# Kernel tuning notes

Hardware: AMD Instinct MI355X
Metric: run time of the kernel (lower is better)

Reference implementation:

```python
import jax, jax.numpy as jnp
import numpy as np

N_NODES = 100000
N_EDGES = 3200000
N_GRAPHS = 512
F_IN = 128
HID = 256
N_LABELS = 10


def setup_inputs() -> dict:
    key = jax.random.key(0)
    ks = jax.random.split(key, 16)
    x = jax.random.normal(ks[0], (N_NODES, F_IN), dtype=jnp.float32)
    edge_index = jax.random.randint(ks[1], (2, N_EDGES), 0, N_NODES)
    batch = jnp.sort(jax.random.randint(ks[2], (N_NODES,), 0, N_GRAPHS))
    dims = [(F_IN, HID), (HID, HID), (HID, HID), (HID, HID // 2), (HID // 2, HID // 2), (HID // 2, HID // 4)]
    inp = {"x": x, "edge_index": edge_index, "batch": batch, "primary_idxs_in_batch": 0}
    for i, (di, do) in enumerate(dims, 1):
        inp[f"W{i}"] = jax.random.normal(ks[2 + i], (di, do), dtype=jnp.float32) * (1.0 / np.sqrt(di))
        inp[f"b{i}"] = jnp.zeros((do,), dtype=jnp.float32)
    inp["Wlin"] = jax.random.normal(ks[12], (HID // 4, N_LABELS), dtype=jnp.float32) * (1.0 / np.sqrt(HID // 4))
    inp["blin"] = jnp.zeros((N_LABELS,), dtype=jnp.float32)
    return inp


def _gcn_conv(h, W, b, src, dst, norm):
    # dense transform first (smaller of the two sides), then normalized scatter-aggregate
    m = (h @ W)[src] * norm[:, None]  # [E+N, C_out]
    return jax.ops.segment_sum(m, dst, num_segments=N_NODES) + b


def reference(x, edge_index, batch, primary_idxs_in_batch,
              W1, b1, W2, b2, W3, b3, W4, b4, W5, b5, W6, b6, Wlin, blin):
    loops = jnp.arange(N_NODES, dtype=edge_index.dtype)
    src = jnp.concatenate([edge_index[0], loops])  # A + I (self loops)
    dst = jnp.concatenate([edge_index[1], loops])
    deg = jax.ops.segment_sum(jnp.ones_like(dst, dtype=x.dtype), dst, num_segments=N_NODES)
    dinv = jnp.where(deg > 0, jax.lax.rsqrt(deg), 0.0)
    norm = dinv[src] * dinv[dst]  # D^-1/2 (A+I) D^-1/2 edge weights

    h = jax.nn.relu(_gcn_conv(x, W1, b1, src, dst, norm))
    h = jax.nn.relu(_gcn_conv(h, W2, b2, src, dst, norm))
    h = jax.nn.relu(_gcn_conv(h, W3, b3, src, dst, norm))
    h = jax.nn.relu(_gcn_conv(h, W4, b4, src, dst, norm))
    h = jax.nn.relu(_gcn_conv(h, W5, b5, src, dst, norm))
    h = _gcn_conv(h, W6, b6, src, dst, norm)

    # primary_idxs_in_batch is falsy (0) -> global_mean_pool path
    s = jax.ops.segment_sum(h, batch, num_segments=N_GRAPHS)
    cnt = jax.ops.segment_sum(jnp.ones((N_NODES,), dtype=h.dtype), batch, num_segments=N_GRAPHS)
    pooled = s / jnp.maximum(cnt, 1.0)[:, None]  # [G, HID//4]

    logits = pooled @ Wlin + blin  # [G, labels]
    return (jax.nn.log_softmax(logits, axis=1), jax.nn.softmax(logits, axis=1))
```

## Files before the change

### kernel.cpp

```cpp
#include <hip/hip_runtime.h>
#include <math.h>

#define NN 100000
#define NE 3200000
#define NG 512
#define NBK 782
#define EBLK 782

typedef __attribute__((ext_vector_type(8))) short short8;
typedef __attribute__((ext_vector_type(4))) float f32x4;
typedef __attribute__((ext_vector_type(2))) float f32x2;

__device__ __forceinline__ float bf2f(unsigned short h){
  return __uint_as_float(((unsigned int)h) << 16);
}
__device__ __forceinline__ unsigned short f2bf(float f){
  unsigned int u = __float_as_uint(f);
  unsigned int r = (u + 0x7fffu + ((u >> 16) & 1u)) >> 16;
  return (unsigned short)r;
}
__device__ __forceinline__ void unpack16(uint4 v, float* f){
  f32x2 p;
  p = __builtin_amdgcn_cvt_pk_f32_fp8(v.x, 0); f[0]=p[0];  f[1]=p[1];
  p = __builtin_amdgcn_cvt_pk_f32_fp8(v.x, 1); f[2]=p[0];  f[3]=p[1];
  p = __builtin_amdgcn_cvt_pk_f32_fp8(v.y, 0); f[4]=p[0];  f[5]=p[1];
  p = __builtin_amdgcn_cvt_pk_f32_fp8(v.y, 1); f[6]=p[0];  f[7]=p[1];
  p = __builtin_amdgcn_cvt_pk_f32_fp8(v.z, 0); f[8]=p[0];  f[9]=p[1];
  p = __builtin_amdgcn_cvt_pk_f32_fp8(v.z, 1); f[10]=p[0]; f[11]=p[1];
  p = __builtin_amdgcn_cvt_pk_f32_fp8(v.w, 0); f[12]=p[0]; f[13]=p[1];
  p = __builtin_amdgcn_cvt_pk_f32_fp8(v.w, 1); f[14]=p[0]; f[15]=p[1];
}
__device__ __forceinline__ unsigned char f2fp8(float v){
  int p = __builtin_amdgcn_cvt_pk_fp8_f32(v, v, 0, 0);
  return (unsigned char)p;
}

__global__ __launch_bounds__(256) void hist2_k(const int* __restrict__ ei,
    int* __restrict__ cnt, int* __restrict__ btot){
  __shared__ int lh[NBK];
  int t = threadIdx.x, b = blockIdx.x;
  for (int i=t; i<NBK; i+=256) lh[i] = 0;
  __syncthreads();
  int base = b*4096;
  #pragma unroll
  for (int u=0; u<16; u++){
    int e = base + u*256 + t;
    if (e < NE) atomicAdd(&lh[ei[NE + e] >> 7], 1);
  }
  __syncthreads();
  for (int i=t; i<NBK; i+=256){
    int v = lh[i];
    cnt[b*NBK + i] = v;
    if (v) atomicAdd(&btot[i], v);
  }
}
__global__ void bscan2_k(const int* __restrict__ btot, int* __restrict__ bptr){
  __shared__ int sc[1024];
  int t = threadIdx.x;
  int v = (t < NBK) ? btot[t] : 0;
  sc[t] = v; __syncthreads();
  for (int off=1; off<1024; off<<=1){
    int u = (t>=off) ? sc[t-off] : 0;
    __syncthreads(); sc[t] += u; __syncthreads();
  }
  if (t < NBK) bptr[t] = sc[t] - v;
  if (t == 1023) bptr[NBK] = sc[1023];
}
__global__ __launch_bounds__(256) void bkpfx_k(int* __restrict__ cnt, const int* __restrict__ bptr){
  __shared__ int sc[256];
  int b = blockIdx.x, t = threadIdx.x;
  int carry = bptr[b];
  for (int base=0; base<EBLK; base+=256){
    int blk = base + t;
    int v = (blk < EBLK) ? cnt[blk*NBK + b] : 0;
    sc[t] = v; __syncthreads();
    for (int off=1; off<256; off<<=1){
      int u = (t>=off) ? sc[t-off] : 0;
      __syncthreads(); sc[t] += u; __syncthreads();
    }
    if (blk < EBLK) cnt[blk*NBK + b] = carry + sc[t] - v;
    carry += sc[255];
    __syncthreads();
  }
}
__global__ __launch_bounds__(256) void scat2_k(const int* __restrict__ ei,
    const int* __restrict__ cnt, unsigned int* __restrict__ ebuf){
  __shared__ int lh[NBK];
  __shared__ int lo[NBK];
  int t = threadIdx.x, b = blockIdx.x;
  for (int i=t; i<NBK; i+=256){ lh[i] = 0; lo[i] = cnt[b*NBK + i]; }
  __syncthreads();
  int base = b*4096;
  #pragma unroll
  for (int u=0; u<16; u++){
    int e = base + u*256 + t;
    if (e < NE){
      int s = ei[e], d = ei[NE + e];
      int bk = d >> 7;
      int r = atomicAdd(&lh[bk], 1);
      ebuf[lo[bk] + r] = (unsigned)s | ((unsigned)(d & 127) << 17);
    }
  }
}
__global__ __launch_bounds__(256) void bcsr_k(const unsigned int* __restrict__ ebuf,
    const int* __restrict__ bptr, int* __restrict__ rp, float* __restrict__ dinv,
    int* __restrict__ col, int* __restrict__ permg){
  __shared__ int cnt[128];
  __shared__ int off[128];
  __shared__ int sc[128];
  __shared__ int dg[128];
  int b = blockIdx.x, t = threadIdx.x;
  int nbase = b << 7;
  int beg = bptr[b], end = bptr[b+1];
  if (t < 128) cnt[t] = 0;
  __syncthreads();
  for (int e = beg + t; e < end; e += 256)
    atomicAdd(&cnt[ebuf[e] >> 17], 1);
  __syncthreads();
  int v = (t < 128) ? cnt[t] : 0;
  if (t < 128){
    sc[t] = v;
    dg[t] = ((nbase + t) < NN) ? v : 0x7FFFFFFF;
  }
  __syncthreads();
  for (int o2=1; o2<128; o2<<=1){
    int u = (t < 128 && t >= o2) ? sc[t-o2] : 0;
    __syncthreads();
    if (t < 128) sc[t] += u;
    __syncthreads();
  }
  if (t < 128){
    int node = nbase + t;
    if (node < NN){
      int ex = beg + sc[t] - v;
      rp[node] = ex;
      off[t] = ex;
      dinv[node] = rsqrtf((float)(v + 1));
      cnt[t] = 0;
    }
    int d = dg[t];
    int rk = 0;
    #pragma unroll 4
    for (int u=0; u<128; u++){
      int du = dg[u];
      rk += (int)((du < d) || (du == d && u < t));
    }
    permg[nbase + rk] = node;
  }
  if (b == ((NN-1) >> 7) && t == 0) rp[NN] = end;
  __syncthreads();
  for (int e = beg + t; e < end; e += 256){
    unsigned int sd = ebuf[e];
    int li = sd >> 17;
    int pos = off[li] + atomicAdd(&cnt[li], 1);
    col[pos] = (int)(sd & 0x1FFFF);
  }
}

__global__ void f2q_k(const float* __restrict__ in, unsigned char* __restrict__ out, int n4){
  int i = blockIdx.x*256 + threadIdx.x;
  if (i < n4){
    float4 v = ((const float4*)in)[i];
    int p = __builtin_amdgcn_cvt_pk_fp8_f32(v.x, v.y, 0, 0);
    p = __builtin_amdgcn_cvt_pk_fp8_f32(v.z, v.w, p, 1);
    ((unsigned int*)out)[i] = (unsigned int)p;
  }
}
__global__ void wswz_all_k(const float* W1, const float* W2, const float* W3,
                           const float* W4, const float* W5, const float* W6,
                           unsigned short* O1, unsigned short* O2, unsigned short* O3,
                           unsigned short* O4, unsigned short* O5, unsigned short* O6){
  int cfg = blockIdx.y;
  int K, N; const float* W; unsigned short* out;
  switch(cfg){
    case 0: K=128; N=256; W=W1; out=O1; break;
    case 1: K=256; N=256; W=W2; out=O2; break;
    case 2: K=256; N=256; W=W3; out=O3; break;
    case 3: K=256; N=128; W=W4; out=O4; break;
    case 4: K=128; N=128; W=W5; out=O5; break;
    default:K=128; N=64;  W=W6; out=O6; break;
  }
  int idx = blockIdx.x*256 + threadIdx.x;
  int total = K*N/8;
  if (idx >= total) return;
  int l = idx & 15;
  int t = idx >> 4; int q = t & 3; t >>= 2;
  int NT = N/16;
  int nt = t % NT, kt = t / NT;
  int kbase = kt*32 + q*8, n = nt*16 + l;
  short8 o;
  #pragma unroll
  for (int j=0;j<8;j++) o[j] = (short)f2bf(W[(size_t)(kbase+j)*N + n]);
  *(short8*)(out + (size_t)idx*8) = o;
}

template<int RS, int W, bool SRC_SCALE, bool RELU, bool HAS_BIAS>
__global__ __launch_bounds__(256) void spmm8_k(const unsigned char* __restrict__ in,
    unsigned short* __restrict__ out,
    const int* __restrict__ rp, const int* __restrict__ col,
    const float* __restrict__ dinv, const int* __restrict__ perm,
    const float* __restrict__ bias)
{
  constexpr int LPR = W/16;
  constexpr int RPW = 64/LPR;
  constexpr int RPB = 4*RPW;
  int tid = threadIdx.x;
  int wv = tid >> 6, lane = tid & 63;
  int sub = lane / LPR, li = lane % LPR;
  int pidx = blockIdx.x*RPB + wv*RPW + sub;
  int row = perm[pidx];
  if (row >= NN) return;
  int beg = rp[row], end = rp[row+1];
  float di = dinv[row];
  int co = blockIdx.y*W + li*16;
  const unsigned char* inb = in + co;
  float acc[16], tmp[16];
  unpack16(*(const uint4*)(inb + (size_t)row*RS), acc);
  if (SRC_SCALE){
    #pragma unroll
    for (int v=0;v<16;v++) acc[v] *= di;
  }
  int j = beg;
  for (; j+8 <= end; j += 8){
    int s[8]; uint4 v[8]; float wgt[8];
    #pragma unroll
    for (int u=0;u<8;u++) s[u] = col[j+u];
    #pragma unroll
    for (int u=0;u<8;u++) v[u] = *(const uint4*)(inb + (size_t)s[u]*RS);
    if (SRC_SCALE){
      #pragma unroll
      for (int u=0;u<8;u++) wgt[u] = dinv[s[u]];
    }
    #pragma unroll
    for (int u=0;u<8;u++){
      unpack16(v[u], tmp);
      float w = SRC_SCALE ? wgt[u] : 1.f;
      #pragma unroll
      for (int vv=0;vv<16;vv++) acc[vv] = fmaf(w, tmp[vv], acc[vv]);
    }
  }
  for (; j < end; j++){
    int ss = col[j];
    uint4 v = *(const uint4*)(inb + (size_t)ss*RS);
    float w = SRC_SCALE ? dinv[ss] : 1.f;
    unpack16(v, tmp);
    #pragma unroll
    for (int vv=0;vv<16;vv++) acc[vv] = fmaf(w, tmp[vv], acc[vv]);
  }
  float bb[16];
  if (HAS_BIAS){
    #pragma unroll
    for (int u=0;u<4;u++) *(float4*)&bb[u*4] = *(const float4*)(bias + co + u*4);
  }
  #pragma unroll
  for (int v=0;v<16;v++){
    acc[v] *= di;
    if (HAS_BIAS) acc[v] += bb[v];
    if (RELU) acc[v] = fmaxf(acc[v], 0.f);
  }
  uint4 o0, o1;
  o0.x = (unsigned int)f2bf(acc[0])  | ((unsigned int)f2bf(acc[1])<<16);
  o0.y = (unsigned int)f2bf(acc[2])  | ((unsigned int)f2bf(acc[3])<<16);
  o0.z = (unsigned int)f2bf(acc[4])  | ((unsigned int)f2bf(acc[5])<<16);
  o0.w = (unsigned int)f2bf(acc[6])  | ((unsigned int)f2bf(acc[7])<<16);
  o1.x = (unsigned int)f2bf(acc[8])  | ((unsigned int)f2bf(acc[9])<<16);
  o1.y = (unsigned int)f2bf(acc[10]) | ((unsigned int)f2bf(acc[11])<<16);
  o1.z = (unsigned int)f2bf(acc[12]) | ((unsigned int)f2bf(acc[13])<<16);
  o1.w = (unsigned int)f2bf(acc[14]) | ((unsigned int)f2bf(acc[15])<<16);
  unsigned short* op = out + (size_t)row*RS + co;
  *(uint4*)op = o0;
  *(uint4*)(op + 8) = o1;
}

template<int K, int N, int EPI>
__global__ __launch_bounds__(256) void mgemm_k(const unsigned short* __restrict__ A,
    const unsigned short* __restrict__ Bsw,
    const float* __restrict__ aux, unsigned short* __restrict__ Cb,
    unsigned char* __restrict__ Cq, int M)
{
  constexpr int NT = 4;
  constexpr int KT = K/32;
  constexpr int NTF = N/16;
  __shared__ short8 Bl[KT*NT*64];
  int tid = threadIdx.x;
  int w = tid >> 6, lane = tid & 63;
  int l = lane & 15, q = lane >> 4;
  int nb0 = blockIdx.x * 64;
  int rb = blockIdx.y*256 + w*64;
  {
    const short8* bsrc = (const short8*)Bsw;
    for (int i = tid; i < KT*NT*64; i += 256){
      int kt = i >> 8;
      int rem = i & 255;
      Bl[i] = bsrc[(kt*NTF + (nb0 >> 4))*64 + rem];
    }
  }
  const unsigned short* ap[4];
  #pragma unroll
  for (int rt=0; rt<4; rt++){
    int r = min(rb + rt*16 + l, M-1);
    ap[rt] = A + (size_t)r*K + q*8;
  }
  f32x4 acc[4][NT];
  #pragma unroll
  for (int rt=0; rt<4; rt++)
    #pragma unroll
    for (int nt=0; nt<NT; nt++) acc[rt][nt] = (f32x4){0,0,0,0};
  short8 a[4], an[4];
  #pragma unroll
  for (int rt=0; rt<4; rt++) a[rt] = *(const short8*)(ap[rt]);
  __syncthreads();
  for (int kt=0; kt<KT; kt++){
    if (kt+1 < KT){
      #pragma unroll
      for (int rt=0; rt<4; rt++) an[rt] = *(const short8*)(ap[rt] + (kt+1)*32);
    }
    const short8* bl = &Bl[kt << 8];
    #pragma unroll
    for (int nt=0; nt<NT; nt++){
      short8 bf = bl[nt*64 + q*16 + l];
      acc[0][nt] = __builtin_amdgcn_mfma_f32_16x16x32_bf16(a[0], bf, acc[0][nt], 0,0,0);
      acc[1][nt] = __builtin_amdgcn_mfma_f32_16x16x32_bf16(a[1], bf, acc[1][nt], 0,0,0);
      acc[2][nt] = __builtin_amdgcn_mfma_f32_16x16x32_bf16(a[2], bf, acc[2][nt], 0,0,0);
      acc[3][nt] = __builtin_amdgcn_mfma_f32_16x16x32_bf16(a[3], bf, acc[3][nt], 0,0,0);
    }
    #pragma unroll
    for (int rt=0; rt<4; rt++) a[rt] = an[rt];
  }
  #pragma unroll
  for (int rt=0; rt<4; rt++){
    int rbb = rb + rt*16;
    #pragma unroll
    for (int nt=0; nt<NT; nt++){
      f32x4 av = acc[rt][nt];
      int n = nb0 + nt*16 + l;
      #pragma unroll
      for (int r=0;r<4;r++){
        int row = rbb + q*4 + r;
        if (row < M){
          float v = av[r];
          if (EPI == 0){
            v = fmaxf(v + aux[n], 0.f);
            Cb[(size_t)row*N + n] = f2bf(v);
          } else {
            v *= aux[row];
            Cq[(size_t)row*N + n] = f2fp8(v);
          }
        }
      }
    }
  }
}

__global__ __launch_bounds__(256) void poolhead_k(const unsigned short* __restrict__ h,
    const int* __restrict__ batch, const float* __restrict__ Wlin,
    const float* __restrict__ blin, float* __restrict__ out)
{
  __shared__ int range[2];
  __shared__ float red[4][64];
  __shared__ float pl[64];
  int g = blockIdx.x;
  if (threadIdx.x < 2){
    int target = g + threadIdx.x;
    int lo = 0, hi = NN;
    while (lo < hi){ int m = (lo+hi) >> 1; if (batch[m] < target) lo = m+1; else hi = m; }
    range[threadIdx.x] = lo;
  }
  __syncthreads();
  int lo = range[0], hi = range[1];
  int ch = threadIdx.x & 63, rg = threadIdx.x >> 6;
  float s = 0.f;
  for (int r = lo + rg; r < hi; r += 4) s += bf2f(h[(size_t)r*64 + ch]);
  red[rg][ch] = s; __syncthreads();
  if (rg == 0){
    float tot = red[0][ch] + red[1][ch] + red[2][ch] + red[3][ch];
    pl[ch] = tot / fmaxf((float)(hi - lo), 1.f);
  }
  __syncthreads();
  if (threadIdx.x == 0){
    float l[10];
    #pragma unroll
    for (int j=0;j<10;j++) l[j] = blin[j];
    for (int c=0;c<64;c++){
      float p = pl[c];
      #pragma unroll
      for (int j=0;j<10;j++) l[j] = fmaf(p, Wlin[c*10 + j], l[j]);
    }
    float mx = l[0];
    #pragma unroll
    for (int j=1;j<10;j++) mx = fmaxf(mx, l[j]);
    float e[10]; float se = 0.f;
    #pragma unroll
    for (int j=0;j<10;j++){ e[j] = expf(l[j]-mx); se += e[j]; }
    float lse = logf(se);
    #pragma unroll
    for (int j=0;j<10;j++){
      out[g*10 + j]         = l[j] - mx - lse;
      out[NG*10 + g*10 + j] = e[j] / se;
    }
  }
}

extern "C" void kernel_launch(void* const* d_in, const int* in_sizes, int n_in,
                              void* d_out, int out_size, void* d_ws, size_t ws_size,
                              hipStream_t stream)
{
  const float* x     = (const float*)d_in[0];
  const int*   ei    = (const int*)  d_in[1];
  const int*   batch = (const int*)  d_in[2];
  const float* W1=(const float*)d_in[4],  *b1=(const float*)d_in[5];
  const float* W2=(const float*)d_in[6],  *b2=(const float*)d_in[7];
  const float* W3=(const float*)d_in[8],  *b3=(const float*)d_in[9];
  const float* W4=(const float*)d_in[10], *b4=(const float*)d_in[11];
  const float* W5=(const float*)d_in[12], *b5=(const float*)d_in[13];
  const float* W6=(const float*)d_in[14], *b6=(const float*)d_in[15];
  const float* Wl=(const float*)d_in[16], *bl=(const float*)d_in[17];
  float* out = (float*)d_out;

  char* ws = (char*)d_ws;
  unsigned short* hA  = (unsigned short*)(ws + 0);
  unsigned short* hB  = (unsigned short*)(ws + 51200000);
  unsigned char*  hQ  = (unsigned char*) (ws + 102400000);
  unsigned char*  xq  = (unsigned char*) (ws + 128000000);
  int*   col   = (int*)  (ws + 140800000);
  unsigned int* ebuf = (unsigned int*)(ws + 153600000);
  int*   rp    = (int*)  (ws + 166400000);
  float* dinv  = (float*)(ws + 166800016);
  unsigned short* W1s = (unsigned short*)(ws + 167200016);
  unsigned short* W2s = (unsigned short*)(ws + 167265552);
  unsigned short* W3s = (unsigned short*)(ws + 167396624);
  unsigned short* W4s = (unsigned short*)(ws + 167527696);
  unsigned short* W5s = (unsigned short*)(ws + 167593232);
  unsigned short* W6s = (unsigned short*)(ws + 167626000);
  int*   btot  = (int*)  (ws + 167642896);
  int*   bptr  = (int*)  (ws + 167646032);
  int*   cnt   = (int*)  (ws + 167649184);
  int*   perm  = cnt;

  hipMemsetAsync(btot, 0, NBK*4, stream);

  hist2_k <<<EBLK, 256, 0, stream>>>(ei, cnt, btot);
  bscan2_k<<<1, 1024, 0, stream>>>(btot, bptr);
  bkpfx_k <<<NBK, 256, 0, stream>>>(cnt, bptr);
  scat2_k <<<EBLK, 256, 0, stream>>>(ei, cnt, ebuf);
  bcsr_k  <<<NBK, 256, 0, stream>>>(ebuf, bptr, rp, dinv, col, perm);

  wswz_all_k<<<dim3(32,6), 256, 0, stream>>>(W1,W2,W3,W4,W5,W6, W1s,W2s,W3s,W4s,W5s,W6s);
  f2q_k<<<(NN*128/4 + 255)/256, 256, 0, stream>>>(x, xq, NN*128/4);

  const int GW128 = (NN + 31)/32;
  const int GW64  = (NN + 63)/64;
  const int GX = (NN + 255)/256;

  spmm8_k<128,128,true,false,false><<<dim3(GW128,1),256,0,stream>>>(xq, hA, rp, col, dinv, perm, nullptr);
  mgemm_k<128,256,0><<<dim3(4,GX),256,0,stream>>>(hA, W1s, b1, hB, nullptr, NN);
  mgemm_k<256,256,1><<<dim3(4,GX),256,0,stream>>>(hB, W2s, dinv, nullptr, hQ, NN);
  spmm8_k<256,128,false,true,true><<<dim3(GW128,2),256,0,stream>>>(hQ, hA, rp, col, dinv, perm, b2);
  mgemm_k<256,256,1><<<dim3(4,GX),256,0,stream>>>(hA, W3s, dinv, nullptr, hQ, NN);
  spmm8_k<256,128,false,true,true><<<dim3(GW128,2),256,0,stream>>>(hQ, hB, rp, col, dinv, perm, b3);
  mgemm_k<256,128,1><<<dim3(2,GX),256,0,stream>>>(hB, W4s, dinv, nullptr, hQ, NN);
  spmm8_k<128,128,false,true,true><<<dim3(GW128,1),256,0,stream>>>(hQ, hA, rp, col, dinv, perm, b4);
  mgemm_k<128,128,1><<<dim3(2,GX),256,0,stream>>>(hA, W5s, dinv, nullptr, hQ, NN);
  spmm8_k<128,128,false,true,true><<<dim3(GW128,1),256,0,stream>>>(hQ, hB, rp, col, dinv, perm, b5);
  mgemm_k<128,64,1><<<dim3(1,GX),256,0,stream>>>(hB, W6s, dinv, nullptr, hQ, NN);
  spmm8_k<64,64,false,false,true><<<dim3(GW64,1),256,0,stream>>>(hQ, hA, rp, col, dinv, perm, b6);

  poolhead_k<<<NG, 256, 0, stream>>>(hA, batch, Wl, bl, out);
}
```

Before: 1.079 ms.

## Interleave SpMM row groups across buckets and use packed fp8 FMA accumulation

The SpMM kernel now maps warps to row groups so that consecutive blocks walk across buckets first and descend the degree-sorted permutation within each bucket, presumably scheduling heavy rows earlier and balancing load. The grid size is derived from the bucket count rather than the node count. The accumulation is rewritten to keep packed f32x2 accumulators and apply elementwise FMA directly on cvt_pk outputs, aiming for packed FMA instructions. The new indexing assumes each bucket has 128 perm slots padded with sentinels, and it risks load imbalance or extra empty warps if that assumption is off.

Result: no change. 1.061 ms (-1.7%).

```diff
diff --git a/kernel.cpp b/kernel.cpp
--- a/kernel.cpp
+++ b/kernel.cpp
@@ -18,17 +18,6 @@
   unsigned int u = __float_as_uint(f);
   unsigned int r = (u + 0x7fffu + ((u >> 16) & 1u)) >> 16;
   return (unsigned short)r;
-}
-__device__ __forceinline__ void unpack16(uint4 v, float* f){
-  f32x2 p;
-  p = __builtin_amdgcn_cvt_pk_f32_fp8(v.x, 0); f[0]=p[0];  f[1]=p[1];
-  p = __builtin_amdgcn_cvt_pk_f32_fp8(v.x, 1); f[2]=p[0];  f[3]=p[1];
-  p = __builtin_amdgcn_cvt_pk_f32_fp8(v.y, 0); f[4]=p[0];  f[5]=p[1];
-  p = __builtin_amdgcn_cvt_pk_f32_fp8(v.y, 1); f[6]=p[0];  f[7]=p[1];
-  p = __builtin_amdgcn_cvt_pk_f32_fp8(v.z, 0); f[8]=p[0];  f[9]=p[1];
-  p = __builtin_amdgcn_cvt_pk_f32_fp8(v.z, 1); f[10]=p[0]; f[11]=p[1];
-  p = __builtin_amdgcn_cvt_pk_f32_fp8(v.w, 0); f[12]=p[0]; f[13]=p[1];
-  p = __builtin_amdgcn_cvt_pk_f32_fp8(v.w, 1); f[14]=p[0]; f[15]=p[1];
 }
 __device__ __forceinline__ unsigned char f2fp8(float v){
   int p = __builtin_amdgcn_cvt_pk_fp8_f32(v, v, 0, 0);
@@ -203,22 +192,35 @@
 {
   constexpr int LPR = W/16;
   constexpr int RPW = 64/LPR;
-  constexpr int RPB = 4*RPW;
+  constexpr int GP  = 128/RPW;
   int tid = threadIdx.x;
   int wv = tid >> 6, lane = tid & 63;
   int sub = lane / LPR, li = lane % LPR;
-  int pidx = blockIdx.x*RPB + wv*RPW + sub;
-  int row = perm[pidx];
+  int G = blockIdx.x*4 + wv;
+  int bucket = G % NBK;
+  int rg = (GP-1) - (G / NBK);
+  int row = perm[(bucket << 7) + rg*RPW + sub];
   if (row >= NN) return;
   int beg = rp[row], end = rp[row+1];
   float di = dinv[row];
   int co = blockIdx.y*W + li*16;
   const unsigned char* inb = in + co;
-  float acc[16], tmp[16];
-  unpack16(*(const uint4*)(inb + (size_t)row*RS), acc);
-  if (SRC_SCALE){
-    #pragma unroll
-    for (int v=0;v<16;v++) acc[v] *= di;
+  f32x2 acc2[8];
+  {
+    uint4 sv = *(const uint4*)(inb + (size_t)row*RS);
+    acc2[0] = __builtin_amdgcn_cvt_pk_f32_fp8(sv.x, 0);
+    acc2[1] = __builtin_amdgcn_cvt_pk_f32_fp8(sv.x, 1);
+    acc2[2] = __builtin_amdgcn_cvt_pk_f32_fp8(sv.y, 0);
+    acc2[3] = __builtin_amdgcn_cvt_pk_f32_fp8(sv.y, 1);
+    acc2[4] = __builtin_amdgcn_cvt_pk_f32_fp8(sv.z, 0);
+    acc2[5] = __builtin_amdgcn_cvt_pk_f32_fp8(sv.z, 1);
+    acc2[6] = __builtin_amdgcn_cvt_pk_f32_fp8(sv.w, 0);
+    acc2[7] = __builtin_amdgcn_cvt_pk_f32_fp8(sv.w, 1);
+    if (SRC_SCALE){
+      f32x2 d2 = (f32x2){di, di};
+      #pragma unroll
+      for (int k=0;k<8;k++) acc2[k] = acc2[k] * d2;
+    }
   }
   int j = beg;
   for (; j+8 <= end; j += 8){
@@ -233,20 +235,35 @@
     }
     #pragma unroll
     for (int u=0;u<8;u++){
-      unpack16(v[u], tmp);
       float w = SRC_SCALE ? wgt[u] : 1.f;
-      #pragma unroll
-      for (int vv=0;vv<16;vv++) acc[vv] = fmaf(w, tmp[vv], acc[vv]);
+      f32x2 w2 = (f32x2){w, w};
+      acc2[0] = __builtin_elementwise_fma(w2, __builtin_amdgcn_cvt_pk_f32_fp8(v[u].x, 0), acc2[0]);
+      acc2[1] = __builtin_elementwise_fma(w2, __builtin_amdgcn_cvt_pk_f32_fp8(v[u].x, 1), acc2[1]);
+      acc2[2] = __builtin_elementwise_fma(w2, __builtin_amdgcn_cvt_pk_f32_fp8(v[u].y, 0), acc2[2]);
+      acc2[3] = __builtin_elementwise_fma(w2, __builtin_amdgcn_cvt_pk_f32_fp8(v[u].y, 1), acc2[3]);
+      acc2[4] = __builtin_elementwise_fma(w2, __builtin_amdgcn_cvt_pk_f32_fp8(v[u].z, 0), acc2[4]);
+      acc2[5] = __builtin_elementwise_fma(w2, __builtin_amdgcn_cvt_pk_f32_fp8(v[u].z, 1), acc2[5]);
+      acc2[6] = __builtin_elementwise_fma(w2, __builtin_amdgcn_cvt_pk_f32_fp8(v[u].w, 0), acc2[6]);
+      acc2[7] = __builtin_elementwise_fma(w2, __builtin_amdgcn_cvt_pk_f32_fp8(v[u].w, 1), acc2[7]);
     }
   }
   for (; j < end; j++){
     int ss = col[j];
     uint4 v = *(const uint4*)(inb + (size_t)ss*RS);
     float w = SRC_SCALE ? dinv[ss] : 1.f;
-    unpack16(v, tmp);
-    #pragma unroll
-    for (int vv=0;vv<16;vv++) acc[vv] = fmaf(w, tmp[vv], acc[vv]);
-  }
+    f32x2 w2 = (f32x2){w, w};
+    acc2[0] = __builtin_elementwise_fma(w2, __builtin_amdgcn_cvt_pk_f32_fp8(v.x, 0), acc2[0]);
+    acc2[1] = __builtin_elementwise_fma(w2, __builtin_amdgcn_cvt_pk_f32_fp8(v.x, 1), acc2[1]);
+    acc2[2] = __builtin_elementwise_fma(w2, __builtin_amdgcn_cvt_pk_f32_fp8(v.y, 0), acc2[2]);
+    acc2[3] = __builtin_elementwise_fma(w2, __builtin_amdgcn_cvt_pk_f32_fp8(v.y, 1), acc2[3]);
+    acc2[4] = __builtin_elementwise_fma(w2, __builtin_amdgcn_cvt_pk_f32_fp8(v.z, 0), acc2[4]);
+    acc2[5] = __builtin_elementwise_fma(w2, __builtin_amdgcn_cvt_pk_f32_fp8(v.z, 1), acc2[5]);
+    acc2[6] = __builtin_elementwise_fma(w2, __builtin_amdgcn_cvt_pk_f32_fp8(v.w, 0), acc2[6]);
+    acc2[7] = __builtin_elementwise_fma(w2, __builtin_amdgcn_cvt_pk_f32_fp8(v.w, 1), acc2[7]);
+  }
+  float acc[16];
+  #pragma unroll
+  for (int k=0;k<8;k++){ acc[2*k] = acc2[k][0]; acc[2*k+1] = acc2[k][1]; }
   float bb[16];
   if (HAS_BIAS){
     #pragma unroll
@@ -448,22 +465,22 @@
   wswz_all_k<<<dim3(32,6), 256, 0, stream>>>(W1,W2,W3,W4,W5,W6, W1s,W2s,W3s,W4s,W5s,W6s);
   f2q_k<<<(NN*128/4 + 255)/256, 256, 0, stream>>>(x, xq, NN*128/4);
 
-  const int GW128 = (NN + 31)/32;
-  const int GW64  = (NN + 63)/64;
-  const int GX = (NN + 255)/256;
-
-  spmm8_k<128,128,true,false,false><<<dim3(GW128,1),256,0,stream>>>(xq, hA, rp, col, dinv, perm, nullptr);
+  const int GX128 = NBK*16/4;
+  const int GX64  = NBK*8/4;
+  const int GX    = (NN + 255)/256;
+
+  spmm8_k<128,128,true,false,false><<<dim3(GX128,1),256,0,stream>>>(xq, hA, rp, col, dinv, perm, nullptr);
   mgemm_k<128,256,0><<<dim3(4,GX),256,0,stream>>>(hA, W1s, b1, hB, nullptr, NN);
   mgemm_k<256,256,1><<<dim3(4,GX),256,0,stream>>>(hB, W2s, dinv, nullptr, hQ, NN);
-  spmm8_k<256,128,false,true,true><<<dim3(GW128,2),256,0,stream>>>(hQ, hA, rp, col, dinv, perm, b2);
+  spmm8_k<256,128,false,true,true><<<dim3(GX128,2),256,0,stream>>>(hQ, hA, rp, col, dinv, perm, b2);
   mgemm_k<256,256,1><<<dim3(4,GX),256,0,stream>>>(hA, W3s, dinv, nullptr, hQ, NN);
-  spmm8_k<256,128,false,true,true><<<dim3(GW128,2),256,0,stream>>>(hQ, hB, rp, col, dinv, perm, b3);
+  spmm8_k<256,128,false,true,true><<<dim3(GX128,2),256,0,stream>>>(hQ, hB, rp, col, dinv, perm, b3);
   mgemm_k<256,128,1><<<dim3(2,GX),256,0,stream>>>(hB, W4s, dinv, nullptr, hQ, NN);
-  spmm8_k<128,128,false,true,true><<<dim3(GW128,1),256,0,stream>>>(hQ, hA, rp, col, dinv, perm, b4);
+  spmm8_k<128,128,false,true,true><<<dim3(GX128,1),256,0,stream>>>(hQ, hA, rp, col, dinv, perm, b4);
   mgemm_k<128,128,1><<<dim3(2,GX),256,0,stream>>>(hA, W5s, dinv, nullptr, hQ, NN);
-  spmm8_k<128,128,false,true,true><<<dim3(GW128,1),256,0,stream>>>(hQ, hB, rp, col, dinv, perm, b5);
+  spmm8_k<128,128,false,true,true><<<dim3(GX128,1),256,0,stream>>>(hQ, hB, rp, col, dinv, perm, b5);
   mgemm_k<128,64,1><<<dim3(1,GX),256,0,stream>>>(hB, W6s, dinv, nullptr, hQ, NN);
-  spmm8_k<64,64,false,false,true><<<dim3(GW64,1),256,0,stream>>>(hQ, hA, rp, col, dinv, perm, b6);
+  spmm8_k<64,64,false,false,true><<<dim3(GX64,1),256,0,stream>>>(hQ, hA, rp, col, dinv, perm, b6);
 
   poolhead_k<<<NG, 256, 0, stream>>>(hA, batch, Wl, bl, out);
 }
```
